# Kernel tuning notes

Measured on AMD Instinct MI355X. Metric: run time of the kernel, lower is better.

The kernel has to match this reference:

```python
import jax, jax.numpy as jnp
import numpy as np

# B=batch, S=seq_len, E=events per example, H=hidden, V=vocab
B, S, E, H, V = 16, 512, 32, 768, 50265


def setup_inputs() -> dict:
    key = jax.random.key(0)
    ks = jax.random.split(key, 12)
    batch_arg = jax.random.randint(ks[0], (B, S), 0, V)
    # distinct event positions per row (the torch loop visits each event once)
    event_pos = jax.vmap(lambda k: jax.random.permutation(k, S)[:E])(
        jax.random.split(ks[1], B))
    mask_indices = event_pos[:, 0]  # ensure the extracted token saw the fusion
    sent_emb = jax.random.normal(ks[2], (B, E, H), dtype=jnp.float32)
    type_emb = jax.random.normal(ks[3], (B, S, H), dtype=jnp.float32)
    emb_table = jax.random.normal(ks[4], (V, H), dtype=jnp.float32) * 0.02
    W1_1 = jax.random.normal(ks[5], (H, H), dtype=jnp.float32) * 0.02
    W1_2 = jax.random.normal(ks[6], (H, H), dtype=jnp.float32) * 0.02
    W2_1 = jax.random.normal(ks[7], (H, H), dtype=jnp.float32) * 0.02
    W2_2 = jax.random.normal(ks[8], (H, H), dtype=jnp.float32) * 0.02
    lm_W = jax.random.normal(ks[9], (H, V), dtype=jnp.float32) * 0.02
    lm_b = jnp.zeros((V,), dtype=jnp.float32)
    return dict(batch_arg=batch_arg, event_pos=event_pos,
                mask_indices=mask_indices, sent_emb=sent_emb,
                type_emb=type_emb, emb_table=emb_table,
                W1_1=W1_1, W1_2=W1_2, W2_1=W2_1, W2_2=W2_2,
                lm_W=lm_W, lm_b=lm_b)


def reference(batch_arg, event_pos, mask_indices, sent_emb, type_emb,
              emb_table, W1_1, W1_2, W2_1, W2_2, lm_W, lm_b):
    # word embedding lookup: [B,S,H]
    word_emb = emb_table[batch_arg]
    bidx = jnp.arange(B)[:, None]
    # gather per-event instance / type embeddings: [B,E,H]
    inst = word_emb[bidx, event_pos]
    typ = type_emb[bidx, event_pos]
    # gate 1: fuse instance with sentence embedding
    g1 = jax.nn.sigmoid(inst @ W1_1 + sent_emb @ W1_2)
    o1 = g1 * inst + (1.0 - g1) * sent_emb
    # gate 2: fuse with type embedding
    g2 = jax.nn.sigmoid(o1 @ W2_1 + typ @ W2_2)
    o2 = g2 * o1 + (1.0 - g2) * typ
    # scatter fused embeddings back into word_emb (positions are distinct)
    word_emb = word_emb.at[bidx, event_pos].set(o2)
    # extract mask-token embedding per example, project to vocab (lm_head)
    mask_emb = word_emb[jnp.arange(B), mask_indices]  # [B,H]
    prediction = mask_emb @ lm_W + lm_b  # [B,V]
    return prediction
```

## Files before the change

### kernel.cpp

```cpp
#include <hip/hip_runtime.h>

#define Hn 768
#define Bn 16
#define Sn 512
#define En 32
#define Vn 50265

#define KC   16
#define KPB  (Hn / KC)
#define VT   1024
#define NVT  50
#define VNP  (NVT * VT)

__global__ __launch_bounds__(256) void gate_layer1(
    const int* __restrict__ batch_arg, const int* __restrict__ event_pos,
    const int* __restrict__ mask_indices, const float* __restrict__ sent_emb,
    const float* __restrict__ emb_table, const float* __restrict__ W1_1,
    const float* __restrict__ W1_2, float* __restrict__ o1_out)
{
    const int b  = blockIdx.x;
    const int j0 = threadIdx.x & 63;
    const int ks = threadIdx.x >> 6;
    const int j  = blockIdx.y * 64 + j0;

    const int mask = mask_indices[b];
    int estar = -1;
    #pragma unroll
    for (int e = 0; e < En; ++e)
        if (event_pos[b * En + e] == mask && estar < 0) estar = e;
    const int tok = batch_arg[b * Sn + mask];

    __shared__ __align__(16) float s_inst[Hn];
    __shared__ __align__(16) float s_sent[Hn];
    for (int t = threadIdx.x; t < Hn; t += 256) {
        s_inst[t] = emb_table[(size_t)tok * Hn + t];
        s_sent[t] = (estar >= 0) ? sent_emb[((size_t)b * En + estar) * Hn + t] : 0.f;
    }
    __syncthreads();

    float a0 = 0.f, a1 = 0.f, c0 = 0.f, c1 = 0.f;
    const float* __restrict__ w1 = W1_1 + (size_t)ks * 192 * Hn + j;
    const float* __restrict__ w2 = W1_2 + (size_t)ks * 192 * Hn + j;
    const float4* __restrict__ si = (const float4*)(s_inst + ks * 192);
    const float4* __restrict__ ss = (const float4*)(s_sent + ks * 192);
    #pragma unroll 4
    for (int k4 = 0; k4 < 48; ++k4) {
        const float4 iv = si[k4];
        const float4 sv = ss[k4];
        const float* __restrict__ wa = w1 + (size_t)k4 * 4 * Hn;
        const float* __restrict__ wb = w2 + (size_t)k4 * 4 * Hn;
        a0 = fmaf(iv.x, wa[0],      a0);
        a1 = fmaf(iv.y, wa[Hn],     a1);
        a0 = fmaf(iv.z, wa[2 * Hn], a0);
        a1 = fmaf(iv.w, wa[3 * Hn], a1);
        c0 = fmaf(sv.x, wb[0],      c0);
        c1 = fmaf(sv.y, wb[Hn],     c1);
        c0 = fmaf(sv.z, wb[2 * Hn], c0);
        c1 = fmaf(sv.w, wb[3 * Hn], c1);
    }

    __shared__ float r_a[4][64];
    __shared__ float r_c[4][64];
    r_a[ks][j0] = a0 + a1; r_c[ks][j0] = c0 + c1;
    __syncthreads();
    if (ks == 0) {
        const float A = r_a[0][j0] + r_a[1][j0] + r_a[2][j0] + r_a[3][j0];
        const float C = r_c[0][j0] + r_c[1][j0] + r_c[2][j0] + r_c[3][j0];
        const float g = 1.f / (1.f + expf(-(A + C)));
        o1_out[b * Hn + j] = g * s_inst[j] + (1.f - g) * s_sent[j];
    }
}

__global__ __launch_bounds__(256) void gate_layer2(
    const int* __restrict__ batch_arg, const int* __restrict__ event_pos,
    const int* __restrict__ mask_indices, const float* __restrict__ type_emb,
    const float* __restrict__ emb_table, const float* __restrict__ W2_1,
    const float* __restrict__ W2_2, const float* __restrict__ o1_in,
    float* __restrict__ me_t)
{
    const int b  = blockIdx.x;
    const int j0 = threadIdx.x & 63;
    const int ks = threadIdx.x >> 6;
    const int j  = blockIdx.y * 64 + j0;

    const int mask = mask_indices[b];
    int estar = -1;
    #pragma unroll
    for (int e = 0; e < En; ++e)
        if (event_pos[b * En + e] == mask && estar < 0) estar = e;
    const int tok = batch_arg[b * Sn + mask];

    __shared__ __align__(16) float s_o1[Hn];
    __shared__ __align__(16) float s_typ[Hn];
    for (int t = threadIdx.x; t < Hn; t += 256) {
        s_o1[t]  = o1_in[b * Hn + t];
        s_typ[t] = type_emb[((size_t)b * Sn + mask) * Hn + t];
    }
    __syncthreads();

    float a0 = 0.f, a1 = 0.f, c0 = 0.f, c1 = 0.f;
    const float* __restrict__ w1 = W2_1 + (size_t)ks * 192 * Hn + j;
    const float* __restrict__ w2 = W2_2 + (size_t)ks * 192 * Hn + j;
    const float4* __restrict__ so = (const float4*)(s_o1  + ks * 192);
    const float4* __restrict__ st = (const float4*)(s_typ + ks * 192);
    #pragma unroll 4
    for (int k4 = 0; k4 < 48; ++k4) {
        const float4 ov = so[k4];
        const float4 tv = st[k4];
        const float* __restrict__ wa = w1 + (size_t)k4 * 4 * Hn;
        const float* __restrict__ wb = w2 + (size_t)k4 * 4 * Hn;
        a0 = fmaf(ov.x, wa[0],      a0);
        a1 = fmaf(ov.y, wa[Hn],     a1);
        a0 = fmaf(ov.z, wa[2 * Hn], a0);
        a1 = fmaf(ov.w, wa[3 * Hn], a1);
        c0 = fmaf(tv.x, wb[0],      c0);
        c1 = fmaf(tv.y, wb[Hn],     c1);
        c0 = fmaf(tv.z, wb[2 * Hn], c0);
        c1 = fmaf(tv.w, wb[3 * Hn], c1);
    }

    __shared__ float r_a[4][64];
    __shared__ float r_c[4][64];
    r_a[ks][j0] = a0 + a1; r_c[ks][j0] = c0 + c1;
    __syncthreads();
    if (ks == 0) {
        const float A = r_a[0][j0] + r_a[1][j0] + r_a[2][j0] + r_a[3][j0];
        const float C = r_c[0][j0] + r_c[1][j0] + r_c[2][j0] + r_c[3][j0];
        const float g = 1.f / (1.f + expf(-(A + C)));
        float o2 = g * s_o1[j] + (1.f - g) * s_typ[j];
        if (estar < 0) o2 = emb_table[(size_t)tok * Hn + j];
        me_t[j * Bn + b] = o2;
    }
}

__global__ __launch_bounds__(256) void lm_head_stream(
    const float* __restrict__ me_t, const float* __restrict__ lm_W,
    float* __restrict__ partial)
{
    __shared__ __align__(16) float s_me[KPB * Bn];

    const int tid = threadIdx.x;
    const int kc  = blockIdx.y;
    const int kb  = kc * KPB;
    const int v0  = blockIdx.x * VT + tid * 4;

    if (tid < KPB * Bn / 4)
        ((float4*)s_me)[tid] = ((const float4*)(me_t + kb * Bn))[tid];
    __syncthreads();

    float4 acc[Bn];
    #pragma unroll
    for (int i = 0; i < Bn; ++i) acc[i] = make_float4(0.f, 0.f, 0.f, 0.f);

#define FMA4(i, s)                                                            \
    acc[i].x = fmaf(s, wv.x, acc[i].x); acc[i].y = fmaf(s, wv.y, acc[i].y);   \
    acc[i].z = fmaf(s, wv.z, acc[i].z); acc[i].w = fmaf(s, wv.w, acc[i].w);

    if (v0 + 3 < Vn) {
        const float* __restrict__ wp = lm_W + (size_t)kb * Vn + v0;
        #pragma unroll 2
        for (int k = 0; k < KPB; ++k) {
            const float4 wv = *(const float4*)(wp + (size_t)k * Vn);
            const float4* __restrict__ m = (const float4*)(s_me + k * Bn);
            const float4 m0 = m[0], m1 = m[1], m2 = m[2], m3 = m[3];
            FMA4(0,  m0.x) FMA4(1,  m0.y) FMA4(2,  m0.z) FMA4(3,  m0.w)
            FMA4(4,  m1.x) FMA4(5,  m1.y) FMA4(6,  m1.z) FMA4(7,  m1.w)
            FMA4(8,  m2.x) FMA4(9,  m2.y) FMA4(10, m2.z) FMA4(11, m2.w)
            FMA4(12, m3.x) FMA4(13, m3.y) FMA4(14, m3.z) FMA4(15, m3.w)
        }
    } else if (v0 < Vn) {
        const float* __restrict__ wq = lm_W + (size_t)kb * Vn + v0;
        for (int k = 0; k < KPB; ++k) {
            const float wx = wq[(size_t)k * Vn];
            #pragma unroll
            for (int b = 0; b < Bn; ++b)
                acc[b].x = fmaf(s_me[k * Bn + b], wx, acc[b].x);
        }
    }
#undef FMA4

    float* __restrict__ pb = partial + (size_t)(kc * Bn) * VNP + v0;
    #pragma unroll
    for (int b = 0; b < Bn; ++b)
        *(float4*)(pb + (size_t)b * VNP) = acc[b];
}

__global__ __launch_bounds__(256) void lm_reduce(
    const float* __restrict__ partial, const float* __restrict__ lm_b,
    float* __restrict__ out)
{
    const int idx = blockIdx.x * 256 + threadIdx.x;
    const int b   = idx / VNP;
    const int v   = idx - b * VNP;
    if (v >= Vn) return;

    float s = 0.f;
    #pragma unroll
    for (int kc = 0; kc < KC; ++kc)
        s += partial[(size_t)(kc * Bn + b) * VNP + v];
    out[(size_t)b * Vn + v] = s + lm_b[v];
}

extern "C" void kernel_launch(void* const* d_in, const int* in_sizes, int n_in,
                              void* d_out, int out_size, void* d_ws, size_t ws_size,
                              hipStream_t stream) {
    const int*   batch_arg    = (const int*)  d_in[0];
    const int*   event_pos    = (const int*)  d_in[1];
    const int*   mask_indices = (const int*)  d_in[2];
    const float* sent_emb     = (const float*)d_in[3];
    const float* type_emb     = (const float*)d_in[4];
    const float* emb_table    = (const float*)d_in[5];
    const float* W1_1         = (const float*)d_in[6];
    const float* W1_2         = (const float*)d_in[7];
    const float* W2_1         = (const float*)d_in[8];
    const float* W2_2         = (const float*)d_in[9];
    const float* lm_W         = (const float*)d_in[10];
    const float* lm_b         = (const float*)d_in[11];
    float* out = (float*)d_out;

    float* o1_ws   = (float*)d_ws;
    float* me_t    = o1_ws + (size_t)Bn * Hn;
    float* partial = me_t  + (size_t)Hn * Bn;

    dim3 g12(Bn, Hn / 64);
    gate_layer1<<<g12, 256, 0, stream>>>(batch_arg, event_pos, mask_indices,
                                         sent_emb, emb_table, W1_1, W1_2, o1_ws);
    gate_layer2<<<g12, 256, 0, stream>>>(batch_arg, event_pos, mask_indices,
                                         type_emb, emb_table, W2_1, W2_2, o1_ws, me_t);

    dim3 gs(NVT, KC);
    lm_head_stream<<<gs, 256, 0, stream>>>(me_t, lm_W, partial);
    lm_reduce<<<(Bn * VNP) / 256, 256, 0, stream>>>(partial, lm_b, out);
}
```

Baseline: 68.67 us.

## Cut lm_head K-split to 4 and software-pipeline weight loads six rows ahead

The lm_head K dimension is now split into 4 chunks instead of 16, so each block does 192 rows. This cuts the partial-sum traffic written by the stream kernel and read back by the reduce kernel. The inner loop keeps six weight float4 rows in flight in registers to hide global-load latency, and launch bounds request 2 blocks per SIMD. The trade-off is only 200 blocks on a large GPU, which lowers parallelism and could leave compute units idle, plus higher register pressure.

```diff
diff --git a/kernel.cpp b/kernel.cpp
--- a/kernel.cpp
+++ b/kernel.cpp
@@ -6,7 +6,7 @@
 #define En 32
 #define Vn 50265
 
-#define KC   16
+#define KC   4
 #define KPB  (Hn / KC)
 #define VT   1024
 #define NVT  50
@@ -133,7 +133,7 @@
     }
 }
 
-__global__ __launch_bounds__(256) void lm_head_stream(
+__global__ __launch_bounds__(256, 2) void lm_head_stream(
     const float* __restrict__ me_t, const float* __restrict__ lm_W,
     float* __restrict__ partial)
 {
@@ -144,8 +144,8 @@
     const int kb  = kc * KPB;
     const int v0  = blockIdx.x * VT + tid * 4;
 
-    if (tid < KPB * Bn / 4)
-        ((float4*)s_me)[tid] = ((const float4*)(me_t + kb * Bn))[tid];
+    for (int i = tid; i < KPB * Bn / 4; i += 256)
+        ((float4*)s_me)[i] = ((const float4*)(me_t + kb * Bn))[i];
     __syncthreads();
 
     float4 acc[Bn];
@@ -156,18 +156,33 @@
     acc[i].x = fmaf(s, wv.x, acc[i].x); acc[i].y = fmaf(s, wv.y, acc[i].y);   \
     acc[i].z = fmaf(s, wv.z, acc[i].z); acc[i].w = fmaf(s, wv.w, acc[i].w);
 
+#define FMAROW(kk, wreg)                                                      \
+    {                                                                         \
+        const float4 wv = wreg;                                               \
+        const float4* __restrict__ m = (const float4*)(s_me + (kk) * Bn);     \
+        const float4 m0 = m[0], m1 = m[1], m2 = m[2], m3 = m[3];              \
+        FMA4(0,  m0.x) FMA4(1,  m0.y) FMA4(2,  m0.z) FMA4(3,  m0.w)          \
+        FMA4(4,  m1.x) FMA4(5,  m1.y) FMA4(6,  m1.z) FMA4(7,  m1.w)          \
+        FMA4(8,  m2.x) FMA4(9,  m2.y) FMA4(10, m2.z) FMA4(11, m2.w)          \
+        FMA4(12, m3.x) FMA4(13, m3.y) FMA4(14, m3.z) FMA4(15, m3.w)          \
+    }
+
     if (v0 + 3 < Vn) {
         const float* __restrict__ wp = lm_W + (size_t)kb * Vn + v0;
-        #pragma unroll 2
-        for (int k = 0; k < KPB; ++k) {
-            const float4 wv = *(const float4*)(wp + (size_t)k * Vn);
-            const float4* __restrict__ m = (const float4*)(s_me + k * Bn);
-            const float4 m0 = m[0], m1 = m[1], m2 = m[2], m3 = m[3];
-            FMA4(0,  m0.x) FMA4(1,  m0.y) FMA4(2,  m0.z) FMA4(3,  m0.w)
-            FMA4(4,  m1.x) FMA4(5,  m1.y) FMA4(6,  m1.z) FMA4(7,  m1.w)
-            FMA4(8,  m2.x) FMA4(9,  m2.y) FMA4(10, m2.z) FMA4(11, m2.w)
-            FMA4(12, m3.x) FMA4(13, m3.y) FMA4(14, m3.z) FMA4(15, m3.w)
+#define LROW(kk) (*(const float4*)(wp + (size_t)(kk) * Vn))
+#define LCL(kk)  LROW((kk) < KPB ? (kk) : (KPB - 1))
+        float4 w0 = LROW(0), w1 = LROW(1), w2 = LROW(2),
+               w3 = LROW(3), w4 = LROW(4), w5 = LROW(5);
+        for (int k0 = 0; k0 < KPB; k0 += 6) {
+            FMAROW(k0 + 0, w0)  w0 = LCL(k0 + 6);
+            FMAROW(k0 + 1, w1)  w1 = LCL(k0 + 7);
+            FMAROW(k0 + 2, w2)  w2 = LCL(k0 + 8);
+            FMAROW(k0 + 3, w3)  w3 = LCL(k0 + 9);
+            FMAROW(k0 + 4, w4)  w4 = LCL(k0 + 10);
+            FMAROW(k0 + 5, w5)  w5 = LCL(k0 + 11);
         }
+#undef LCL
+#undef LROW
     } else if (v0 < Vn) {
         const float* __restrict__ wq = lm_W + (size_t)kb * Vn + v0;
         for (int k = 0; k < KPB; ++k) {
@@ -177,12 +192,15 @@
                 acc[b].x = fmaf(s_me[k * Bn + b], wx, acc[b].x);
         }
     }
+#undef FMAROW
 #undef FMA4
 
-    float* __restrict__ pb = partial + (size_t)(kc * Bn) * VNP + v0;
-    #pragma unroll
-    for (int b = 0; b < Bn; ++b)
-        *(float4*)(pb + (size_t)b * VNP) = acc[b];
+    if (v0 < Vn) {
+        float* __restrict__ pb = partial + (size_t)(kc * Bn) * VNP + v0;
+        #pragma unroll
+        for (int b = 0; b < Bn; ++b)
+            *(float4*)(pb + (size_t)b * VNP) = acc[b];
+    }
 }
 
 __global__ __launch_bounds__(256) void lm_reduce(
@@ -230,5 +248,5 @@
 
     dim3 gs(NVT, KC);
     lm_head_stream<<<gs, 256, 0, stream>>>(me_t, lm_W, partial);
-    lm_reduce<<<(Bn * VNP) / 256, 256, 0, stream>>>(partial, lm_b, out);
-}
+    lm_reduce<<<(Bn * VNP + 255) / 256, 256, 0, stream>>>(partial, lm_b, out);
+}
```

New measurement: 75.47 us. 9.9% more time.
